# Kernel tuning notes

Measured on AMD Instinct MI355X. Metric: run time of the kernel, lower is better.

Reference implementation:

```python
import jax, jax.numpy as jnp
import numpy as np

B, Q, K, H = 4, 128, 1024, 256
QS, KS, DV = 256, 256, 256


def setup_inputs() -> dict:
    key = jax.random.key(0)
    k1, k2, k3, k4, k5, k6, k7 = jax.random.split(key, 7)
    return {
        "queries": jax.random.normal(k1, (B, Q, QS), dtype=jnp.float32),
        "keys": jax.random.normal(k2, (B, K, KS), dtype=jnp.float32),
        "values": jax.random.normal(k3, (B, K, DV), dtype=jnp.float32),
        "valid_lens": jax.random.randint(k4, (B,), 1, K, dtype=jnp.int64),
        "Wq": jax.random.normal(k5, (QS, H), dtype=jnp.float32) / np.sqrt(QS),
        "Wk": jax.random.normal(k6, (KS, H), dtype=jnp.float32) / np.sqrt(KS),
        "Wv": jax.random.normal(k7, (H,), dtype=jnp.float32) / np.sqrt(H),
    }


def reference(queries, keys, values, valid_lens, Wq, Wk, Wv):
    # Projections: [B,Q,H] and [B,K,H]
    q = jnp.einsum("bqe,eh->bqh", queries, Wq)
    k = jnp.einsum("bke,eh->bkh", keys, Wk)
    # Broadcast add + tanh: [B,Q,K,H] intermediate (the kernel-headroom op)
    feats = jnp.tanh(q[:, :, None, :] + k[:, None, :, :])
    # hidden -> 1 reduction: scores [B,Q,K]
    scores = jnp.einsum("bqkh,h->bqk", feats, Wv)
    # masked softmax: positions >= valid_len set to -1e6 (as in sequence_mask)
    mask = jnp.arange(scores.shape[-1])[None, None, :] < valid_lens[:, None, None]
    scores = jnp.where(mask, scores, jnp.float32(-1e6))
    attn = jax.nn.softmax(scores, axis=-1)
    # dropout is identity in eval mode
    return jnp.einsum("bqk,bkv->bqv", attn, values)
```

## Files before the change

### kernel.cpp

```cpp
#include <hip/hip_runtime.h>

#define NB 4
#define NQ 128
#define NK 1024
#define NH 256
#define NE 256
#define NV 256

#define TSCALE 2.8853900817779268f
#define LOG2E  1.4426950408889634f

static __device__ __forceinline__ float fexp2(float x){ return __builtin_amdgcn_exp2f(x); }
static __device__ __forceinline__ float frcp (float x){ return __builtin_amdgcn_rcpf(x); }
static __device__ __forceinline__ float tanh_of(float x){
    float e = fexp2(x * TSCALE);
    return fmaf(-2.0f, frcp(e + 1.0f), 1.0f);
}

__global__ __launch_bounds__(256) void proj_kernel(
    const float* __restrict__ qin, const float* __restrict__ kin,
    const float* __restrict__ Wq, const float* __restrict__ Wk,
    const float* __restrict__ Wv,
    float4* __restrict__ qTa, float4* __restrict__ kTt) {
    const int tid = threadIdx.x;
    const int bi  = blockIdx.x;
    __shared__ float tr[NH][9];
    if (bi < NB * 32) {
        const int row0 = bi * 4;
        const float* r0 = qin + row0 * NE;
        float a0 = 0.f, a1 = 0.f, a2 = 0.f, a3 = 0.f;
#pragma unroll 2
        for (int e = 0; e < NE; e += 4) {
            float4 q0 = *(const float4*)(r0 + e);
            float4 q1 = *(const float4*)(r0 + NE + e);
            float4 q2 = *(const float4*)(r0 + 2 * NE + e);
            float4 q3 = *(const float4*)(r0 + 3 * NE + e);
#pragma unroll
            for (int j = 0; j < 4; ++j) {
                float w = Wq[(e + j) * NH + tid];
                a0 = fmaf(((const float*)&q0)[j], w, a0);
                a1 = fmaf(((const float*)&q1)[j], w, a1);
                a2 = fmaf(((const float*)&q2)[j], w, a2);
                a3 = fmaf(((const float*)&q3)[j], w, a3);
            }
        }
        qTa[bi * NH + tid] = make_float4(tanh_of(a0), tanh_of(a1),
                                         tanh_of(a2), tanh_of(a3));
    } else {
        const int kb = bi - NB * 32;
        const int b  = kb >> 7;
        const int k0 = (kb & 127) * 8;
        const int c   = k0 >> 6;
        const int kl0 = k0 & 63;
        const float* kr = kin + (b * NK + k0) * NE;
        float acc[8] = {0.f,0.f,0.f,0.f,0.f,0.f,0.f,0.f};
#pragma unroll 2
        for (int e = 0; e < NE; e += 4) {
            float4 kvv[8];
#pragma unroll
            for (int i = 0; i < 8; ++i) kvv[i] = *(const float4*)(kr + i * NE + e);
#pragma unroll
            for (int j = 0; j < 4; ++j) {
                float w = Wk[(e + j) * NH + tid];
#pragma unroll
                for (int i = 0; i < 8; ++i)
                    acc[i] = fmaf(((const float*)&kvv[i])[j], w, acc[i]);
            }
        }
#pragma unroll
        for (int i = 0; i < 8; ++i) tr[tid][i] = tanh_of(acc[i]);
        __syncthreads();
#pragma unroll
        for (int p = 0; p < 2; ++p) {
            int idx2 = p * 256 + tid;
            int hg = idx2 >> 3;
            int kk = idx2 & 7;
            float4 v = make_float4(tr[hg*4+0][kk], tr[hg*4+1][kk],
                                   tr[hg*4+2][kk], tr[hg*4+3][kk]);
            kTt[((b * 16 + c) * 64 + hg) * 64 + kl0 + kk] = v;
        }
    }
}

__global__ __launch_bounds__(256) void attn_kernel(
    const float4* __restrict__ qTa,
    const float4* __restrict__ kTt, const float* __restrict__ V,
    const int* __restrict__ vlen, const float4* __restrict__ Wv4,
    float* __restrict__ part_m, float* __restrict__ part_s,
    float* __restrict__ part_pv) {
    const int tid = threadIdx.x, lane = tid & 63, wvid = tid >> 6;
    const int n0 = (vlen[0] + 63) >> 6, n1 = (vlen[1] + 63) >> 6;
    const int n2 = (vlen[2] + 63) >> 6, n3 = (vlen[3] + 63) >> 6;
    const int G  = n0 + n1 + n2 + n3;
    const int bi = blockIdx.x;
    const int xcd = bi & 7;
    const int jj  = bi >> 3;
    const int qq  = jj & 31;
    const int gs  = ((jj >> 5) << 3) + xcd;
    if (gs >= G) return;
    int b, chunk;
    if      (gs < n0)           { b = 0; chunk = gs; }
    else if (gs < n0 + n1)      { b = 1; chunk = gs - n0; }
    else if (gs < n0 + n1 + n2) { b = 2; chunk = gs - n0 - n1; }
    else                        { b = 3; chunk = gs - n0 - n1 - n2; }
    const int vl    = vlen[b];
    const int k0    = chunk * 64;
    const int k     = k0 + lane;
    const int pidx  = (b * 32 + qq) * 16 + chunk;
    float* pm  = part_m + pidx * 4;
    float* ps  = part_s + pidx * 4;
    float* ppv = part_pv + pidx * (4 * NV);

    __shared__ float red17[4][64 * 17];
    __shared__ float pwT[64][4];
    __shared__ float4 qL[NH];

    qL[tid] = qTa[(b * 32 + qq) * NH + tid];
    __syncthreads();

    const float4* kp = kTt + ((b * 16 + chunk) * 64 + wvid * 16) * 64 + lane;
    float acc0 = 0.f, acc1 = 0.f, acc2 = 0.f, acc3 = 0.f;
#pragma unroll
    for (int i = 0; i < 16; ++i) {
        float4 kv4 = kp[i * 64];
        const int h4 = wvid * 16 + i;
        float4 wv4 = Wv4[h4];
#pragma unroll
        for (int j = 0; j < 4; ++j) {
            float kv  = (j==0)?kv4.x:(j==1)?kv4.y:(j==2)?kv4.z:kv4.w;
            float wvj = (j==0)?wv4.x:(j==1)?wv4.y:(j==2)?wv4.z:wv4.w;
            float4 qa = qL[h4 * 4 + j];
            float p0 = fmaf(qa.x, kv, 1.0f), t0 = qa.x + kv;
            float p1 = fmaf(qa.y, kv, 1.0f), t1 = qa.y + kv;
            float p2 = fmaf(qa.z, kv, 1.0f), t2 = qa.z + kv;
            float p3 = fmaf(qa.w, kv, 1.0f), t3 = qa.w + kv;
            float ab = p0 * p1, cd = p2 * p3;
            float rw = wvj * frcp(ab * cd);
            float rab = rw * cd, rcd = rw * ab;
            acc0 = fmaf(t0, rab * p1, acc0);
            acc1 = fmaf(t1, rab * p0, acc1);
            acc2 = fmaf(t2, rcd * p3, acc2);
            acc3 = fmaf(t3, rcd * p2, acc3);
        }
    }
    {
        float* hp = &red17[wvid][lane * 17];
        hp[0] = acc0; hp[1] = acc1; hp[2] = acc2; hp[3] = acc3;
    }
    __syncthreads();
    {
        const int row = wvid;
        float s = red17[0][lane * 17 + row] + red17[1][lane * 17 + row]
                + red17[2][lane * 17 + row] + red17[3][lane * 17 + row];
        s = (k < vl) ? s : -1e30f;
        float m = s;
#pragma unroll
        for (int d = 32; d >= 1; d >>= 1) m = fmaxf(m, __shfl_xor(m, d, 64));
        float p = fexp2((s - m) * LOG2E);
        float u = p;
#pragma unroll
        for (int d = 32; d >= 1; d >>= 1) u += __shfl_xor(u, d, 64);
        if (lane == 0) { pm[row] = m; ps[row] = u; }
        pwT[lane][row] = p;
    }
    __syncthreads();
    {
        const float* Vb = V + (b * NK + k0) * NV;
        const int v4 = lane * 4;
        float4 o0 = {0,0,0,0}, o1 = {0,0,0,0}, o2 = {0,0,0,0}, o3 = {0,0,0,0};
#pragma unroll 4
        for (int kk = 0; kk < 16; ++kk) {
            const int kkk = wvid * 16 + kk;
            float4 pv = *(const float4*)&pwT[kkk][0];
            float4 vv = *(const float4*)&Vb[kkk * NV + v4];
            o0.x = fmaf(pv.x, vv.x, o0.x); o0.y = fmaf(pv.x, vv.y, o0.y);
            o0.z = fmaf(pv.x, vv.z, o0.z); o0.w = fmaf(pv.x, vv.w, o0.w);
            o1.x = fmaf(pv.y, vv.x, o1.x); o1.y = fmaf(pv.y, vv.y, o1.y);
            o1.z = fmaf(pv.y, vv.z, o1.z); o1.w = fmaf(pv.y, vv.w, o1.w);
            o2.x = fmaf(pv.z, vv.x, o2.x); o2.y = fmaf(pv.z, vv.y, o2.y);
            o2.z = fmaf(pv.z, vv.z, o2.z); o2.w = fmaf(pv.z, vv.w, o2.w);
            o3.x = fmaf(pv.w, vv.x, o3.x); o3.y = fmaf(pv.w, vv.y, o3.y);
            o3.z = fmaf(pv.w, vv.z, o3.z); o3.w = fmaf(pv.w, vv.w, o3.w);
        }
        float* pd = &red17[wvid][lane * 17];
        *(float4*)(pd + 0)  = o0;
        *(float4*)(pd + 4)  = o1;
        *(float4*)(pd + 8)  = o2;
        *(float4*)(pd + 12) = o3;
    }
    __syncthreads();
    {
        const int row = tid >> 6, vg = tid & 63;
        float4 r = {0,0,0,0};
#pragma unroll
        for (int ww = 0; ww < 4; ++ww) {
            float4 t = *(const float4*)&red17[ww][vg * 17 + row * 4];
            r.x += t.x; r.y += t.y; r.z += t.z; r.w += t.w;
        }
        *(float4*)&ppv[row * NV + vg * 4] = r;
    }
}

__global__ __launch_bounds__(256) void combine_kernel(
    const float* __restrict__ part_m, const float* __restrict__ part_s,
    const float* __restrict__ part_pv, const int* __restrict__ vlen,
    float* __restrict__ out) {
    const int tid = threadIdx.x;
    const int idx = blockIdx.x;
    const int bi  = idx >> 2;
    const int i   = idx & 3;
    const int b   = bi >> 5;
    const int nb  = (vlen[b] + 63) >> 6;
    const int base = bi * 16;
    float M = -1e30f;
    for (int q = 0; q < nb; ++q)
        M = fmaxf(M, part_m[(base + q) * 4 + i]);
    float S = 0.f, o = 0.f;
    for (int q = 0; q < nb; ++q) {
        float wq = fexp2((part_m[(base + q) * 4 + i] - M) * LOG2E);
        S = fmaf(part_s[(base + q) * 4 + i], wq, S);
        o = fmaf(part_pv[((base + q) * 4 + i) * NV + tid], wq, o);
    }
    out[(bi * 4 + i) * NV + tid] = o * frcp(S);
}

extern "C" void kernel_launch(void* const* d_in, const int* in_sizes, int n_in,
                              void* d_out, int out_size, void* d_ws, size_t ws_size,
                              hipStream_t stream) {
    const float* queries = (const float*)d_in[0];
    const float* keys    = (const float*)d_in[1];
    const float* values  = (const float*)d_in[2];
    const int*   vlens   = (const int*)  d_in[3];
    const float* Wq      = (const float*)d_in[4];
    const float* Wk      = (const float*)d_in[5];
    const float* Wv      = (const float*)d_in[6];
    float* out = (float*)d_out;

    float4* qTa    = (float4*)d_ws;
    float4* kTt    = qTa + NB * 32 * NH;
    float*  part_m = (float*)(kTt + NB * 64 * NK);
    float*  part_s = part_m + 8192;
    float*  part_pv = part_s + 8192;

    proj_kernel   <<<dim3(640), dim3(256), 0, stream>>>(queries, keys, Wq, Wk, Wv,
                                                        qTa, kTt);
    attn_kernel   <<<dim3(2048), dim3(256), 0, stream>>>(qTa, kTt, values,
                                                         vlens, (const float4*)Wv,
                                                         part_m, part_s, part_pv);
    combine_kernel<<<dim3(512), dim3(256), 0, stream>>>(part_m, part_s, part_pv,
                                                        vlens, out);
}
```

Before: 114.8 us.

## Fuse split-K combine into attention kernel via last-block atomic counter

Removes the separate combine kernel launch by having each attention block increment a per-(batch,query-group) atomic counter after writing its partials; the last-arriving block performs the max/rescale/sum combine and writes the output. Counters are zeroed in the projection kernel. This saves a launch and a pass over partials at the cost of threadfences, an atomic per block, and a serialized tail combine in one block per group.

```diff
diff --git a/kernel.cpp b/kernel.cpp
--- a/kernel.cpp
+++ b/kernel.cpp
@@ -21,10 +21,12 @@
     const float* __restrict__ qin, const float* __restrict__ kin,
     const float* __restrict__ Wq, const float* __restrict__ Wk,
     const float* __restrict__ Wv,
-    float4* __restrict__ qTa, float4* __restrict__ kTt) {
+    float4* __restrict__ qTa, float4* __restrict__ kTt,
+    int* __restrict__ counters) {
     const int tid = threadIdx.x;
     const int bi  = blockIdx.x;
     __shared__ float tr[NH][9];
+    if (bi == 0 && tid < 128) counters[tid] = 0;
     if (bi < NB * 32) {
         const int row0 = bi * 4;
         const float* r0 = qin + row0 * NE;
@@ -87,7 +89,8 @@
     const float4* __restrict__ kTt, const float* __restrict__ V,
     const int* __restrict__ vlen, const float4* __restrict__ Wv4,
     float* __restrict__ part_m, float* __restrict__ part_s,
-    float* __restrict__ part_pv) {
+    float* __restrict__ part_pv, int* __restrict__ counters,
+    float* __restrict__ out) {
     const int tid = threadIdx.x, lane = tid & 63, wvid = tid >> 6;
     const int n0 = (vlen[0] + 63) >> 6, n1 = (vlen[1] + 63) >> 6;
     const int n2 = (vlen[2] + 63) >> 6, n3 = (vlen[3] + 63) >> 6;
@@ -104,9 +107,11 @@
     else if (gs < n0 + n1 + n2) { b = 2; chunk = gs - n0 - n1; }
     else                        { b = 3; chunk = gs - n0 - n1 - n2; }
     const int vl    = vlen[b];
+    const int nb    = (vl + 63) >> 6;
     const int k0    = chunk * 64;
     const int k     = k0 + lane;
-    const int pidx  = (b * 32 + qq) * 16 + chunk;
+    const int gidx  = b * 32 + qq;
+    const int pidx  = gidx * 16 + chunk;
     float* pm  = part_m + pidx * 4;
     float* ps  = part_s + pidx * 4;
     float* ppv = part_pv + pidx * (4 * NV);
@@ -114,8 +119,9 @@
     __shared__ float red17[4][64 * 17];
     __shared__ float pwT[64][4];
     __shared__ float4 qL[NH];
-
-    qL[tid] = qTa[(b * 32 + qq) * NH + tid];
+    __shared__ int lastflag;
+
+    qL[tid] = qTa[gidx * NH + tid];
     __syncthreads();
 
     const float4* kp = kTt + ((b * 16 + chunk) * 64 + wvid * 16) * 64 + lane;
@@ -199,29 +205,29 @@
         }
         *(float4*)&ppv[row * NV + vg * 4] = r;
     }
-}
-
-__global__ __launch_bounds__(256) void combine_kernel(
-    const float* __restrict__ part_m, const float* __restrict__ part_s,
-    const float* __restrict__ part_pv, const int* __restrict__ vlen,
-    float* __restrict__ out) {
-    const int tid = threadIdx.x;
-    const int idx = blockIdx.x;
-    const int bi  = idx >> 2;
-    const int i   = idx & 3;
-    const int b   = bi >> 5;
-    const int nb  = (vlen[b] + 63) >> 6;
-    const int base = bi * 16;
-    float M = -1e30f;
-    for (int q = 0; q < nb; ++q)
-        M = fmaxf(M, part_m[(base + q) * 4 + i]);
-    float S = 0.f, o = 0.f;
-    for (int q = 0; q < nb; ++q) {
-        float wq = fexp2((part_m[(base + q) * 4 + i] - M) * LOG2E);
-        S = fmaf(part_s[(base + q) * 4 + i], wq, S);
-        o = fmaf(part_pv[((base + q) * 4 + i) * NV + tid], wq, o);
-    }
-    out[(bi * 4 + i) * NV + tid] = o * frcp(S);
+
+    __threadfence();
+    if (tid == 0) {
+        int prev = atomicAdd(&counters[gidx], 1);
+        lastflag = (prev == nb - 1);
+    }
+    __syncthreads();
+    if (!lastflag) return;
+    __threadfence();
+    const int base = gidx * 16;
+#pragma unroll
+    for (int i = 0; i < 4; ++i) {
+        float M = -1e30f;
+        for (int q = 0; q < nb; ++q)
+            M = fmaxf(M, part_m[(base + q) * 4 + i]);
+        float S = 0.f, o = 0.f;
+        for (int q = 0; q < nb; ++q) {
+            float wq = fexp2((part_m[(base + q) * 4 + i] - M) * LOG2E);
+            S = fmaf(part_s[(base + q) * 4 + i], wq, S);
+            o = fmaf(part_pv[((base + q) * 4 + i) * NV + tid], wq, o);
+        }
+        out[(gidx * 4 + i) * NV + tid] = o * frcp(S);
+    }
 }
 
 extern "C" void kernel_launch(void* const* d_in, const int* in_sizes, int n_in,
@@ -241,12 +247,12 @@
     float*  part_m = (float*)(kTt + NB * 64 * NK);
     float*  part_s = part_m + 8192;
     float*  part_pv = part_s + 8192;
-
-    proj_kernel   <<<dim3(640), dim3(256), 0, stream>>>(queries, keys, Wq, Wk, Wv,
-                                                        qTa, kTt);
-    attn_kernel   <<<dim3(2048), dim3(256), 0, stream>>>(qTa, kTt, values,
-                                                         vlens, (const float4*)Wv,
-                                                         part_m, part_s, part_pv);
-    combine_kernel<<<dim3(512), dim3(256), 0, stream>>>(part_m, part_s, part_pv,
-                                                        vlens, out);
-}
+    int*    counters = (int*)(part_pv + 2097152);
+
+    proj_kernel<<<dim3(640), dim3(256), 0, stream>>>(queries, keys, Wq, Wk, Wv,
+                                                     qTa, kTt, counters);
+    attn_kernel<<<dim3(2048), dim3(256), 0, stream>>>(qTa, kTt, values,
+                                                      vlens, (const float4*)Wv,
+                                                      part_m, part_s, part_pv,
+                                                      counters, out);
+}
```

New measurement: 256.8 us. 124% more time.
